# Kernel optimization log

Measured on AMD Instinct MI355X. Metric: run time of the kernel, lower is better.

Reference implementation:

```python
import jax, jax.numpy as jnp
import numpy as np
import math

D_MODEL = 1024
NHEADS = 16
HEAD_DIM = D_MODEL // NHEADS


def make_pe(n, d):
    # sinusoidal positional encoding table, shape [n, d]
    pos = jnp.arange(n, dtype=jnp.float32)[:, None]
    div = jnp.exp(jnp.arange(0, d, 2, dtype=jnp.float32) * (-math.log(10000.0) / d))
    pe = jnp.zeros((n, d), dtype=jnp.float32)
    pe = pe.at[:, 0::2].set(jnp.sin(pos * div))
    pe = pe.at[:, 1::2].set(jnp.cos(pos * div))
    return pe


def setup_inputs() -> dict:
    key = jax.random.key(0)
    ks = jax.random.split(key, 6)
    B, S, D = 2, 2048, D_MODEL
    x = jax.random.normal(ks[0], (B, S, D), dtype=jnp.float32)
    mask = jax.random.randint(ks[1], (1, 1, S, S), 0, 2, dtype=jnp.int32)
    qkv_w = jax.random.normal(ks[2], (3 * D, D), dtype=jnp.float32) * (1.0 / math.sqrt(D))
    qkv_b = jax.random.normal(ks[3], (3 * D,), dtype=jnp.float32) * 0.02
    fc_w = jax.random.normal(ks[4], (D, D), dtype=jnp.float32) * (1.0 / math.sqrt(D))
    fc_b = jax.random.normal(ks[5], (D,), dtype=jnp.float32) * 0.02
    return {"x": x, "mask": mask, "qkv_w": qkv_w, "qkv_b": qkv_b, "fc_w": fc_w, "fc_b": fc_b}


def reference(x, mask, qkv_w, qkv_b, fc_w, fc_b):
    B, S, D = x.shape
    H, Hd = NHEADS, HEAD_DIM
    qkv = jnp.einsum('bsd,ed->bse', x, qkv_w) + qkv_b  # [B,S,3D]
    xq, xk, xv = jnp.split(qkv, 3, axis=-1)
    # Faithful to source: pe[:x.size(0)] slices batch_size rows, broadcast over seq dim
    pe = make_pe(B, D)[:, None, :]  # [B,1,D]
    xq = xq + pe
    xk = xk + pe
    # [B,S,D] -> [B,H,S,Hd]
    xq = xq.reshape(B, S, H, Hd).transpose(0, 2, 1, 3)
    xk = xk.reshape(B, S, H, Hd).transpose(0, 2, 1, 3)
    xv = xv.reshape(B, S, H, Hd).transpose(0, 2, 1, 3)
    scores = jnp.einsum('bhqd,bhkd->bhqk', xq, xk) / math.sqrt(Hd)
    scores = jnp.where(mask == 1, jnp.float32(-1e9), scores)
    probs = jax.nn.softmax(scores, axis=-1)
    out = jnp.einsum('bhqk,bhkd->bhqd', probs, xv)
    out = out.transpose(0, 2, 1, 3).reshape(B, S, D)
    return jnp.einsum('bsd,ed->bse', out, fc_w) + fc_b
```

## Files before the change

kernel.cpp:

```cpp
#include <hip/hip_runtime.h>
#include <hip/hip_bf16.h>
#include <cstdint>

typedef __attribute__((ext_vector_type(8))) short short8;
typedef __attribute__((ext_vector_type(4))) float f32x4;
typedef __attribute__((ext_vector_type(16))) float f32x16;
typedef __attribute__((ext_vector_type(4))) unsigned uint4v;

#define DEV static __device__ __forceinline__

DEV f32x4 mfma16(short8 a, short8 b, f32x4 c) {
    return __builtin_amdgcn_mfma_f32_16x16x32_bf16(a, b, c, 0, 0, 0);
}
DEV f32x16 mfma32(short8 a, short8 b, f32x16 c) {
    return __builtin_amdgcn_mfma_f32_32x32x16_bf16(a, b, c, 0, 0, 0);
}

DEV unsigned short f2bf(float f) {
    __hip_bfloat16 h = __float2bfloat16(f);
    return __builtin_bit_cast(unsigned short, h);
}

DEV float fexp2(float x) {
#if __has_builtin(__builtin_amdgcn_exp2f)
    return __builtin_amdgcn_exp2f(x);
#else
    float r;
    asm("v_exp_f32 %0, %1" : "=v"(r) : "v"(x));
    return r;
#endif
}

DEV unsigned cvtpk(float lo, float hi) {
    unsigned r;
    asm("v_cvt_pk_bf16_f32 %0, %1, %2" : "=v"(r) : "v"(lo), "v"(hi));
    return r;
}
DEV void plswap(unsigned& a, unsigned& b) {
    asm volatile("v_permlane32_swap_b32 %0, %1" : "+v"(a), "+v"(b));
}

#define GLOAD16(gp, lp)                                                        \
    __builtin_amdgcn_global_load_lds(                                          \
        (const __attribute__((address_space(1))) unsigned int*)(uintptr_t)(gp),\
        (__attribute__((address_space(3))) unsigned int*)(uintptr_t)(lp),      \
        16, 0, 0)

__global__ void prep(const float* __restrict__ x, const float* __restrict__ wq,
                     const float* __restrict__ wf, const int* __restrict__ mask,
                     unsigned short* __restrict__ xb, unsigned short* __restrict__ wqb,
                     unsigned short* __restrict__ wfb, unsigned int* __restrict__ wT,
                     float* __restrict__ pe) {
    const int bid = blockIdx.x;
    if (bid < 8192) {
        int i = bid * 256 + threadIdx.x;
        const float* src; unsigned short* dst; int off;
        if (i < 1048576)      { src = x;  dst = xb;  off = i; }
        else if (i < 1835008) { src = wq; dst = wqb; off = i - 1048576; }
        else                  { src = wf; dst = wfb; off = i - 1835008; }
        float4 v = ((const float4*)src)[off];
        ushort4 o;
        o.x = f2bf(v.x); o.y = f2bf(v.y); o.z = f2bf(v.z); o.w = f2bf(v.w);
        ((ushort4*)dst)[off] = o;
    } else if (bid < 8704) {
        int o = (bid - 8192) * 256 + threadIdx.x;
        int kb = o >> 11, row = o & 2047;
        const int4* m4 = (const int4*)(mask + (size_t)row * 2048 + kb * 32);
        unsigned int bits = 0;
#pragma unroll
        for (int j = 0; j < 8; j++) {
            int4 v = m4[j];
            bits |= (unsigned)(v.x & 1) << (4 * j);
            bits |= (unsigned)(v.y & 1) << (4 * j + 1);
            bits |= (unsigned)(v.z & 1) << (4 * j + 2);
            bits |= (unsigned)(v.w & 1) << (4 * j + 3);
        }
        wT[o] = bits;
    } else {
        for (int i = threadIdx.x; i < 512; i += 256) {
            float div = expf((float)(2 * i) * (-9.210340371976184f / 1024.0f));
            pe[2 * i]          = 0.0f;
            pe[2 * i + 1]      = 1.0f;
            pe[1024 + 2 * i]     = sinf(div);
            pe[1024 + 2 * i + 1] = cosf(div);
        }
    }
}

DEV void gemm_mainloop(const unsigned short* __restrict__ A,
                       const unsigned short* __restrict__ Bm,
                       int m0, int n0, f32x4 (&acc)[4][4],
                       unsigned short* As, unsigned short* Bs) {
    const int t = threadIdx.x;
    const int w = t >> 6;
    const int l = t & 63, lr = l & 15, lg = l >> 4;
    const int wr = w >> 1, wc = w & 1;
    const int srow = t >> 2;
    const int scg = ((t & 3) ^ ((t >> 3) & 3)) * 8;
#pragma unroll
    for (int i = 0; i < 4; i++)
#pragma unroll
        for (int j = 0; j < 4; j++) acc[i][j] = f32x4{0.f, 0.f, 0.f, 0.f};

    const unsigned short* Ap = A + (size_t)(m0 + srow) * 1024 + scg;
    const unsigned short* Bp = Bm + (size_t)(n0 + srow) * 1024 + scg;
    unsigned short* dA = As + w * 512;
    unsigned short* dB = Bs + w * 512;

    const int slot = (lg ^ ((lr >> 1) & 3)) * 8;
    const unsigned short* Ar = As + (wr * 64 + lr) * 32 + slot;
    const unsigned short* Br = Bs + (wc * 64 + lr) * 32 + slot;

#define STAGE(buf, k0)                                                \
    {                                                                 \
        GLOAD16(Ap + (k0), dA + (buf) * 4096);                        \
        GLOAD16(Ap + 64 * 1024 + (k0), dA + (buf) * 4096 + 2048);     \
        GLOAD16(Bp + (k0), dB + (buf) * 4096);                        \
        GLOAD16(Bp + 64 * 1024 + (k0), dB + (buf) * 4096 + 2048);     \
    }

    STAGE(0, 0);
#pragma unroll 2
    for (int k0 = 0; k0 < 1024; k0 += 32) {
        const int cur = (k0 >> 5) & 1;
        __syncthreads();
        if (k0 + 32 < 1024) STAGE(cur ^ 1, k0 + 32);
        short8 af[4], bfr[4];
#pragma unroll
        for (int i = 0; i < 4; i++)
            af[i] = *(const short8*)(Ar + cur * 4096 + i * 512);
#pragma unroll
        for (int j = 0; j < 4; j++)
            bfr[j] = *(const short8*)(Br + cur * 4096 + j * 512);
#pragma unroll
        for (int i = 0; i < 4; i++)
#pragma unroll
            for (int j = 0; j < 4; j++)
                acc[i][j] = mfma16(af[i], bfr[j], acc[i][j]);
    }
#undef STAGE
}

__global__ __launch_bounds__(256) void qkv_gemm(
    const unsigned short* __restrict__ x, const unsigned short* __restrict__ wq,
    const float* __restrict__ bias, const float* __restrict__ pe,
    unsigned short* __restrict__ qo, unsigned short* __restrict__ ko,
    unsigned short* __restrict__ vt) {
    __shared__ unsigned short SB[16384];
    const int lin = blockIdx.x;
    const int swz = (lin & 7) * 96 + (lin >> 3);
    const int m0 = (swz / 24) * 128, n0 = (swz % 24) * 128;
    f32x4 acc[4][4];
    gemm_mainloop(x, wq, m0, n0, acc, SB, SB + 8192);

    const int t = threadIdx.x, w = t >> 6, l = t & 63;
    const int wr = w >> 1, wc = w & 1, lr = l & 15, lg = l >> 4;
    const int part = n0 >> 10;
    const int h0 = (n0 & 1023) >> 6;
    const int b  = m0 >> 11;

    __syncthreads();
#pragma unroll
    for (int i = 0; i < 4; i++) {
#pragma unroll
        for (int j = 0; j < 4; j++) {
            const int n = n0 + wc * 64 + j * 16 + lr;
            const int d = n & 1023, hd = d & 63;
            const int h_loc = (d >> 6) & 1;
            const float bia = bias[n];
            const float pv = (part < 2) ? pe[b * 1024 + d] : 0.f;
#pragma unroll
            for (int r = 0; r < 4; r++) {
                const int m = m0 + wr * 64 + i * 16 + lg * 4 + r;
                const int s = m & 2047, s5 = s & 31, t_loc = (s >> 5) & 3;
                float v = acc[i][j][r] + bia;
                int inner;
                if (part == 2) {
                    inner = (hd >> 5) * 1024 + ((s5 >> 4) & 1) * 512 +
                            (((s5 >> 3) & 1) * 32 + (hd & 31)) * 8 + (s5 & 7);
                } else {
                    v += pv;
                    if (part == 0) v *= 0.1803368801111204f;
                    inner = (hd >> 4) * 512 + (((hd >> 3) & 1) * 32 + s5) * 8 + (hd & 7);
                }
                SB[(t_loc * 2 + h_loc) * 2048 + inner] = f2bf(v);
            }
        }
    }
    __syncthreads();

    unsigned short* dst0 = (part == 0) ? qo : (part == 1) ? ko : vt;
    const int cidx = t >> 5;
    const int t_g = ((m0 & 2047) >> 5) + (cidx >> 1);
    const int bh = b * 16 + h0 + (cidx & 1);
    unsigned short* gdst = dst0 + (size_t)bh * 131072 + t_g * 2048 + (t & 31) * 64;
    const unsigned short* lsrc = SB + cidx * 2048 + (t & 31) * 64;
#pragma unroll
    for (int u = 0; u < 8; u++)
        *(short8*)(gdst + u * 8) = *(const short8*)(lsrc + u * 8);
}

__global__ __launch_bounds__(256) void fc_gemm(
    const unsigned short* __restrict__ a, const unsigned short* __restrict__ wf,
    const float* __restrict__ bias, float* __restrict__ out) {
    __shared__ unsigned short As[2 * 2048], Bs[2 * 4096];
    const int lin = blockIdx.x;
    const int swz = (lin & 7) * 64 + (lin >> 3);
    const int m0 = (swz >> 3) * 64, n0 = (swz & 7) * 128;

    const int t = threadIdx.x;
    const int w = t >> 6;
    const int l = t & 63, lr = l & 15, lg = l >> 4;
    const int wr = w >> 1, wc = w & 1;
    const int srow = t >> 2;
    const int scg = ((t & 3) ^ ((t >> 3) & 3)) * 8;
    f32x4 acc[2][4];
#pragma unroll
    for (int i = 0; i < 2; i++)
#pragma unroll
        for (int j = 0; j < 4; j++) acc[i][j] = f32x4{0.f, 0.f, 0.f, 0.f};

    const unsigned short* Ap = a + (size_t)(m0 + srow) * 1024 + scg;
    const unsigned short* Bp = wf + (size_t)(n0 + srow) * 1024 + scg;
    unsigned short* dA = As + w * 512;
    unsigned short* dB = Bs + w * 512;

    const int slot = (lg ^ ((lr >> 1) & 3)) * 8;
    const unsigned short* Ar = As + (wr * 32 + lr) * 32 + slot;
    const unsigned short* Br = Bs + (wc * 64 + lr) * 32 + slot;

#define STAGE(buf, k0)                                                \
    {                                                                 \
        GLOAD16(Ap + (k0), dA + (buf) * 2048);                        \
        GLOAD16(Bp + (k0), dB + (buf) * 4096);                        \
        GLOAD16(Bp + 64 * 1024 + (k0), dB + (buf) * 4096 + 2048);     \
    }

    STAGE(0, 0);
#pragma unroll 2
    for (int k0 = 0; k0 < 1024; k0 += 32) {
        const int cur = (k0 >> 5) & 1;
        __syncthreads();
        if (k0 + 32 < 1024) STAGE(cur ^ 1, k0 + 32);
        short8 af[2], bfr[4];
#pragma unroll
        for (int i = 0; i < 2; i++)
            af[i] = *(const short8*)(Ar + cur * 2048 + i * 512);
#pragma unroll
        for (int j = 0; j < 4; j++)
            bfr[j] = *(const short8*)(Br + cur * 4096 + j * 512);
#pragma unroll
        for (int i = 0; i < 2; i++)
#pragma unroll
            for (int j = 0; j < 4; j++)
                acc[i][j] = mfma16(af[i], bfr[j], acc[i][j]);
    }
#undef STAGE

#pragma unroll
    for (int i = 0; i < 2; i++) {
#pragma unroll
        for (int j = 0; j < 4; j++) {
            const int n = n0 + wc * 64 + j * 16 + lr;
            const float bia = bias[n];
#pragma unroll
            for (int r = 0; r < 4; r++) {
                const int m = m0 + wr * 32 + i * 16 + lg * 4 + r;
                out[(size_t)m * 1024 + n] = acc[i][j][r] + bia;
            }
        }
    }
}

__global__ __launch_bounds__(256, 3) void attn(
    const unsigned short* __restrict__ q, const unsigned short* __restrict__ k,
    const unsigned short* __restrict__ vt, const unsigned int* __restrict__ mw,
    unsigned short* __restrict__ ao) {
    __shared__ float CL[4][2080];
    const int t = threadIdx.x, w = t >> 6;
    const int l = t & 63, c = l & 31, hi = l >> 5;
    const int bid = blockIdx.x;
    const int xcd = bid & 7, idx = bid >> 3;
    const int bh = xcd * 4 + (idx & 3);
    const int qpair = idx >> 2;
    const int chunk = w & 1;
    const int qb = qpair * 2 + (w >> 1);
    const int b = bh >> 4, h = bh & 15;
    const int kb0 = chunk * 32;

    const unsigned short* qfb = q + (size_t)bh * 131072 + qb * 2048 + l * 8;
    const unsigned short* kfb = k + (size_t)bh * 131072 + l * 8;
    const unsigned short* vfb = vt + (size_t)bh * 131072 + l * 8;

    short8 qf[4];
#pragma unroll
    for (int d = 0; d < 4; d++)
        qf[d] = *(const short8*)(qfb + d * 512);

    float z = 0.f;
    asm volatile("" : "+v"(z));
    f32x16 FZ;
#pragma unroll
    for (int i = 0; i < 16; i++) FZ[i] = z;

    f32x16 OT0, OT1;
#pragma unroll
    for (int i = 0; i < 16; i++) { OT0[i] = 0.f; OT1[i] = 0.f; }
    float lrow = 0.f;

#pragma unroll 4
    for (int kb = kb0; kb < kb0 + 32; kb++) {
        const unsigned short* kp = kfb + kb * 2048;
        const unsigned short* vp = vfb + kb * 2048;
        short8 kf[4], vf[2][2];
#pragma unroll
        for (int d = 0; d < 4; d++) kf[d] = *(const short8*)(kp + d * 512);
#pragma unroll
        for (int kc = 0; kc < 2; kc++) {
            vf[0][kc] = *(const short8*)(vp + kc * 512);
            vf[1][kc] = *(const short8*)(vp + 1024 + kc * 512);
        }
        const unsigned int wd = mw[kb * 2048 + qb * 32 + c];

        __builtin_amdgcn_s_setprio(1);
        f32x16 S = mfma32(kf[0], qf[0], FZ);
#pragma unroll
        for (int d = 1; d < 4; d++) S = mfma32(kf[d], qf[d], S);
        __builtin_amdgcn_s_setprio(0);

        const unsigned int wds = wd >> (4 * hi);
        float p[16];
#pragma unroll
        for (int g = 0; g < 4; g++)
#pragma unroll
            for (int u = 0; u < 4; u++)
                p[g * 4 + u] = (wds & (1u << (8 * g + u))) ? -1e9f : S[g * 4 + u];
#pragma unroll
        for (int i = 0; i < 16; i++) p[i] = fexp2(p[i]);

        float rs = (((p[0] + p[1]) + (p[2] + p[3])) + ((p[4] + p[5]) + (p[6] + p[7]))) +
                   (((p[8] + p[9]) + (p[10] + p[11])) + ((p[12] + p[13]) + (p[14] + p[15])));
        rs += __shfl_xor(rs, 32);
        lrow += rs;

        unsigned w8[8];
#pragma unroll
        for (int g = 0; g < 4; g++) {
            w8[2 * g]     = cvtpk(p[4 * g], p[4 * g + 1]);
            w8[2 * g + 1] = cvtpk(p[4 * g + 2], p[4 * g + 3]);
        }
        short8 pa[2];
#pragma unroll
        for (int kc = 0; kc < 2; kc++) {
            unsigned a0 = w8[4 * kc], a2 = w8[4 * kc + 2];
            plswap(a0, a2);
            unsigned a1 = w8[4 * kc + 1], a3 = w8[4 * kc + 3];
            plswap(a1, a3);
            uint4v tv; tv[0] = a0; tv[1] = a1; tv[2] = a2; tv[3] = a3;
            pa[kc] = __builtin_bit_cast(short8, tv);
        }

        __builtin_amdgcn_s_setprio(1);
        OT0 = mfma32(vf[0][0], pa[0], OT0);
        OT0 = mfma32(vf[0][1], pa[1], OT0);
        OT1 = mfma32(vf[1][0], pa[0], OT1);
        OT1 = mfma32(vf[1][1], pa[1], OT1);
        __builtin_amdgcn_s_setprio(0);
    }

    float* R = CL[w];
#pragma unroll
    for (int i = 0; i < 16; i++) {
        const int kr = (i & 3) + 8 * (i >> 2) + 4 * hi;
        R[kr * 32 + c]        = OT0[i];
        R[(32 + kr) * 32 + c] = OT1[i];
    }
    if (hi == 0) R[2048 + c] = lrow;
    __syncthreads();

    const float* C0 = CL[(w >> 1) * 2];
    const float* C1 = CL[(w >> 1) * 2 + 1];
    const int qq = l >> 1, db = (l & 1) * 16 + (w & 1) * 32;
    const float inv = 1.0f / (C0[2048 + qq] + C1[2048 + qq]);
    const int row = b * 2048 + (qpair * 2 + (w >> 1)) * 32 + qq;
    unsigned short* gout = ao + (size_t)row * 1024 + h * 64 + db;
    uint4v pk0, pk1;
#pragma unroll
    for (int u = 0; u < 4; u++) {
        const int d0 = db + 2 * u, d1 = db + 8 + 2 * u;
        pk0[u] = cvtpk((C0[d0 * 32 + qq] + C1[d0 * 32 + qq]) * inv,
                       (C0[(d0 + 1) * 32 + qq] + C1[(d0 + 1) * 32 + qq]) * inv);
        pk1[u] = cvtpk((C0[d1 * 32 + qq] + C1[d1 * 32 + qq]) * inv,
                       (C0[(d1 + 1) * 32 + qq] + C1[(d1 + 1) * 32 + qq]) * inv);
    }
    *(uint4v*)(gout)     = pk0;
    *(uint4v*)(gout + 8) = pk1;
}

extern "C" void kernel_launch(void* const* d_in, const int* in_sizes, int n_in,
                              void* d_out, int out_size, void* d_ws, size_t ws_size,
                              hipStream_t stream) {
    const float* x     = (const float*)d_in[0];
    const int*   mask  = (const int*)d_in[1];
    const float* qkv_w = (const float*)d_in[2];
    const float* qkv_b = (const float*)d_in[3];
    const float* fc_w  = (const float*)d_in[4];
    const float* fc_b  = (const float*)d_in[5];
    float* out = (float*)d_out;

    char* ws = (char*)d_ws;
    size_t off = 0;
    auto alloc = [&](size_t bytes) {
        off = (off + 255) & ~(size_t)255;
        void* p = ws + off;
        off += bytes;
        return p;
    };
    float*          pe     = (float*)alloc(2 * 1024 * 4);
    unsigned int*   mwords = (unsigned int*)alloc((size_t)2048 * 64 * 4);
    unsigned short* xb     = (unsigned short*)alloc((size_t)4096 * 1024 * 2);
    unsigned short* wqkv   = (unsigned short*)alloc((size_t)3072 * 1024 * 2);
    unsigned short* wfc    = (unsigned short*)alloc((size_t)1024 * 1024 * 2);
    unsigned short* qb16   = (unsigned short*)alloc((size_t)2 * 16 * 2048 * 64 * 2);
    unsigned short* kb16   = (unsigned short*)alloc((size_t)2 * 16 * 2048 * 64 * 2);
    unsigned short* vtb    = (unsigned short*)alloc((size_t)2 * 16 * 64 * 2048 * 2);
    unsigned short* attn_o = (unsigned short*)alloc((size_t)4096 * 1024 * 2);

    prep<<<dim3(8705), 256, 0, stream>>>(x, qkv_w, fc_w, mask, xb, wqkv, wfc, mwords, pe);
    qkv_gemm<<<dim3(768), 256, 0, stream>>>(xb, wqkv, qkv_b, pe, qb16, kb16, vtb);
    attn<<<dim3(1024), 256, 0, stream>>>(qb16, kb16, vtb, mwords, attn_o);
    fc_gemm<<<dim3(512), 256, 0, stream>>>(attn_o, wfc, fc_b, out);
}
```

Baseline: 139.0 us.

## Split attention keys four ways per query block and double the grid

Each attention block now handles a single 32-row query block, and its four waves each process a quarter of the keys instead of two query blocks with two key halves each. Partial outputs and row sums are merged through shared memory in two phases: two waves write, the other two add. The grid doubles to 2048 blocks and shared memory per block halves. The aim is more parallelism, shorter per-wave loops and better occupancy, at the cost of an extra barrier and a read-modify-write merge step per block.

```diff
diff --git a/kernel.cpp b/kernel.cpp
--- a/kernel.cpp
+++ b/kernel.cpp
@@ -276,17 +276,15 @@
     const unsigned short* __restrict__ q, const unsigned short* __restrict__ k,
     const unsigned short* __restrict__ vt, const unsigned int* __restrict__ mw,
     unsigned short* __restrict__ ao) {
-    __shared__ float CL[4][2080];
+    __shared__ float CL[2][2080];
     const int t = threadIdx.x, w = t >> 6;
     const int l = t & 63, c = l & 31, hi = l >> 5;
     const int bid = blockIdx.x;
     const int xcd = bid & 7, idx = bid >> 3;
     const int bh = xcd * 4 + (idx & 3);
-    const int qpair = idx >> 2;
-    const int chunk = w & 1;
-    const int qb = qpair * 2 + (w >> 1);
+    const int qb = idx >> 2;
     const int b = bh >> 4, h = bh & 15;
-    const int kb0 = chunk * 32;
+    const int kb0 = w * 16;
 
     const unsigned short* qfb = q + (size_t)bh * 131072 + qb * 2048 + l * 8;
     const unsigned short* kfb = k + (size_t)bh * 131072 + l * 8;
@@ -309,7 +307,7 @@
     float lrow = 0.f;
 
 #pragma unroll 4
-    for (int kb = kb0; kb < kb0 + 32; kb++) {
+    for (int kb = kb0; kb < kb0 + 16; kb++) {
         const unsigned short* kp = kfb + kb * 2048;
         const unsigned short* vp = vfb + kb * 2048;
         short8 kf[4], vf[2][2];
@@ -368,33 +366,41 @@
         __builtin_amdgcn_s_setprio(0);
     }
 
-    float* R = CL[w];
-#pragma unroll
-    for (int i = 0; i < 16; i++) {
-        const int kr = (i & 3) + 8 * (i >> 2) + 4 * hi;
-        R[kr * 32 + c]        = OT0[i];
-        R[(32 + kr) * 32 + c] = OT1[i];
-    }
-    if (hi == 0) R[2048 + c] = lrow;
+    float* R = CL[w & 1];
+    if (w < 2) {
+#pragma unroll
+        for (int i = 0; i < 16; i++) {
+            const int kr = (i & 3) + 8 * (i >> 2) + 4 * hi;
+            R[kr * 32 + c]        = OT0[i];
+            R[(32 + kr) * 32 + c] = OT1[i];
+        }
+        if (hi == 0) R[2048 + c] = lrow;
+    }
     __syncthreads();
-
-    const float* C0 = CL[(w >> 1) * 2];
-    const float* C1 = CL[(w >> 1) * 2 + 1];
-    const int qq = l >> 1, db = (l & 1) * 16 + (w & 1) * 32;
-    const float inv = 1.0f / (C0[2048 + qq] + C1[2048 + qq]);
-    const int row = b * 2048 + (qpair * 2 + (w >> 1)) * 32 + qq;
-    unsigned short* gout = ao + (size_t)row * 1024 + h * 64 + db;
-    uint4v pk0, pk1;
+    if (w >= 2) {
+#pragma unroll
+        for (int i = 0; i < 16; i++) {
+            const int kr = (i & 3) + 8 * (i >> 2) + 4 * hi;
+            R[kr * 32 + c]        += OT0[i];
+            R[(32 + kr) * 32 + c] += OT1[i];
+        }
+        if (hi == 0) R[2048 + c] += lrow;
+    }
+    __syncthreads();
+
+    const int qq = l >> 1, d0 = w * 16 + (l & 1) * 8;
+    const float inv = 1.0f / (CL[0][2048 + qq] + CL[1][2048 + qq]);
+    const int row = b * 2048 + qb * 32 + qq;
+    unsigned short* gout = ao + (size_t)row * 1024 + h * 64 + d0;
+    uint4v pk;
 #pragma unroll
     for (int u = 0; u < 4; u++) {
-        const int d0 = db + 2 * u, d1 = db + 8 + 2 * u;
-        pk0[u] = cvtpk((C0[d0 * 32 + qq] + C1[d0 * 32 + qq]) * inv,
-                       (C0[(d0 + 1) * 32 + qq] + C1[(d0 + 1) * 32 + qq]) * inv);
-        pk1[u] = cvtpk((C0[d1 * 32 + qq] + C1[d1 * 32 + qq]) * inv,
-                       (C0[(d1 + 1) * 32 + qq] + C1[(d1 + 1) * 32 + qq]) * inv);
-    }
-    *(uint4v*)(gout)     = pk0;
-    *(uint4v*)(gout + 8) = pk1;
+        const int d = d0 + 2 * u;
+        float a0 = CL[0][d * 32 + qq]       + CL[1][d * 32 + qq];
+        float a1 = CL[0][(d + 1) * 32 + qq] + CL[1][(d + 1) * 32 + qq];
+        pk[u] = cvtpk(a0 * inv, a1 * inv);
+    }
+    *(uint4v*)gout = pk;
 }
 
 extern "C" void kernel_launch(void* const* d_in, const int* in_sizes, int n_in,
@@ -428,6 +434,6 @@
 
     prep<<<dim3(8705), 256, 0, stream>>>(x, qkv_w, fc_w, mask, xb, wqkv, wfc, mwords, pe);
     qkv_gemm<<<dim3(768), 256, 0, stream>>>(xb, wqkv, qkv_b, pe, qb16, kb16, vtb);
-    attn<<<dim3(1024), 256, 0, stream>>>(qb16, kb16, vtb, mwords, attn_o);
+    attn<<<dim3(2048), 256, 0, stream>>>(qb16, kb16, vtb, mwords, attn_o);
     fc_gemm<<<dim3(512), 256, 0, stream>>>(attn_o, wfc, fc_b, out);
 }
```

New measurement: 136.5 us, median of 2. About the same (-1.8%).
